# Kernel tuning notes

Measured on AMD Instinct MI355X. Metric: run time of the kernel, lower is better.

The kernel has to match this reference:

```python
import jax, jax.numpy as jnp
import numpy as np


def _chain_edges(n):
    # bidirectional chain edges + self loops (PyG GATConv add_self_loops=True default)
    src = np.concatenate([np.arange(n - 1), np.arange(1, n), np.arange(n)])
    dst = np.concatenate([np.arange(1, n), np.arange(n - 1), np.arange(n)])
    return jnp.asarray(src), jnp.asarray(dst)


def _gat(x, W, a_src, a_dst, bias, src, dst, n, heads, ch, concat):
    # x: [B, n, Fin]; PyG GATConv v1 math (lin has no bias, bias added post-agg)
    B = x.shape[0]
    xh = (x @ W).reshape(B, n, heads, ch)  # [B,n,h,c]
    es = jnp.einsum('bnhc,hc->bnh', xh, a_src)
    ed = jnp.einsum('bnhc,hc->bnh', xh, a_dst)
    e = jax.nn.leaky_relu(es[:, src] + ed[:, dst], 0.2)  # [B,E,h]
    e = jnp.moveaxis(e, 1, 0)                            # [E,B,h]
    m = jax.ops.segment_max(e, dst, num_segments=n)      # scatter-softmax over incoming edges
    w = jnp.exp(e - m[dst])
    denom = jax.ops.segment_sum(w, dst, num_segments=n)
    alpha = w / denom[dst]                               # [E,B,h]
    msgs = alpha[..., None] * jnp.moveaxis(xh[:, src], 1, 0)  # [E,B,h,c]
    out = jnp.moveaxis(jax.ops.segment_sum(msgs, dst, num_segments=n), 0, 1)  # [B,n,h,c]
    out = out.reshape(B, n, heads * ch) if concat else out.mean(axis=2)
    return out + bias


def _mlp(x, w1, b1, w2, b2, w3, b3):
    h = jax.nn.leaky_relu(x @ w1 + b1, 0.01)
    h = jax.nn.leaky_relu(h @ w2 + b2, 0.01)
    return h @ w3 + b3


def setup_inputs() -> dict:
    key = jax.random.key(0)
    ks = jax.random.split(key, 21)
    B, n, d_state, hid, da = 2048, 50, 64, 128, 4
    r = lambda k, shp, s: (jax.random.normal(k, shp, dtype=jnp.float32) * s)
    return {
        'state': r(ks[0], (B, n, d_state), 1.0),
        'W1': r(ks[1], (d_state, 2 * hid), 0.1), 'att_src1': r(ks[2], (2, hid), 0.1),
        'att_dst1': r(ks[3], (2, hid), 0.1), 'b1': r(ks[4], (2 * hid,), 0.02),
        'W2': r(ks[5], (2 * hid, hid), 0.1), 'att_src2': r(ks[6], (1, hid), 0.1),
        'att_dst2': r(ks[7], (1, hid), 0.1), 'b2': r(ks[8], (hid,), 0.02),
        'aw1': r(ks[9], (hid, 128), 0.1), 'ab1': r(ks[10], (128,), 0.02),
        'aw2': r(ks[11], (128, 128), 0.1), 'ab2': r(ks[12], (128,), 0.02),
        'aw3': r(ks[13], (128, da), 0.1), 'ab3': r(ks[14], (da,), 0.02),
        'vw1': r(ks[15], (hid, 128), 0.1), 'vb1': r(ks[16], (128,), 0.02),
        'vw2': r(ks[17], (128, 128), 0.1), 'vb2': r(ks[18], (128,), 0.02),
        'vw3': r(ks[19], (128, 1), 0.1), 'vb3': r(ks[20], (1,), 0.02),
    }


def reference(state, W1, att_src1, att_dst1, b1, W2, att_src2, att_dst2, b2,
              aw1, ab1, aw2, ab2, aw3, ab3, vw1, vb1, vw2, vb2, vw3, vb3):
    B, n, _ = state.shape
    src, dst = _chain_edges(n)
    x = jax.nn.gelu(_gat(state, W1, att_src1, att_dst1, b1, src, dst, n, 2, 128, True), approximate=False)
    x = jax.nn.gelu(_gat(x, W2, att_src2, att_dst2, b2, src, dst, n, 1, 128, False), approximate=False)
    graph_emb = x.mean(axis=1)                      # global_mean_pool over chain nodes
    value = _mlp(graph_emb, vw1, vb1, vw2, vb2, vw3, vb3)   # [B,1]
    mean = _mlp(x, aw1, ab1, aw2, ab2, aw3, ab3).reshape(B, -1)  # [B, n*d_action]
    return mean, value
```

## Files before the change

### kernel.cpp

```cpp
#include <hip/hip_runtime.h>

#define DI __device__ __forceinline__

typedef unsigned int uint32;
typedef unsigned short u16;
typedef __attribute__((ext_vector_type(8))) short s8v;
typedef __attribute__((ext_vector_type(4))) float f4v;

DI float lrelu(float x, float s){ return x > 0.f ? x : s*x; }
DI float fastrcp(float x){ float r; asm("v_rcp_f32 %0, %1" : "=v"(r) : "v"(x)); return r; }
DI u16 f2bu(float f){ uint32 u = __float_as_uint(f); return (u16)((u + 0x7FFFu + ((u>>16)&1u)) >> 16); }
DI float b16f(u16 u){ return __uint_as_float(((uint32)u)<<16); }

DI float gelu_f(float x){
  const float z = fabsf(x) * 0.70710678118654752f;
  const float t = fastrcp(1.f + 0.3275911f*z);
  float p = 1.061405429f;
  p = p*t - 1.453152027f;
  p = p*t + 1.421413741f;
  p = p*t - 0.284496736f;
  p = p*t + 0.254829592f;
  p = p*t;
  const float e = __expf(-z*z);
  float er = 1.f - p*e;
  er = copysignf(er, x);
  return 0.5f*x*(1.f + er);
}

DI f4v mfma16(s8v a, s8v b, f4v c){
  return __builtin_amdgcn_mfma_f32_16x16x32_bf16(a, b, c, 0, 0, 0);
}

constexpr int NNODE = 50;
constexpr int NT = 512;
constexpr int SCS = 266;

constexpr int WS1  = 0;
constexpr int WS2  = 17408;
constexpr int WSA1 = 54272;
constexpr int WSA2 = 70656;
constexpr int WSA3 = 87040;
constexpr int WSTOT= 89088;

__global__ __launch_bounds__(256)
void ac_prep(const float* __restrict__ w1, const float* __restrict__ as1, const float* __restrict__ ad1,
             const float* __restrict__ w2, const float* __restrict__ as2, const float* __restrict__ ad2,
             const float* __restrict__ aw1, const float* __restrict__ aw2, const float* __restrict__ aw3,
             u16* __restrict__ ws)
{
  const int T1 = 272*64, T2 = 144*256, T3 = 128*128;
  for (int t = blockIdx.x*blockDim.x + threadIdx.x; t < WSTOT; t += gridDim.x*blockDim.x){
    float v; int o;
    if (t < T1){
      int n = t>>6, k = t&63;
      if (n < 256) v = w1[k*256 + n];
      else if (n < 260){
        int sd = (n-256)>>1, h = (n-256)&1;
        const float* av = (sd ? ad1 : as1) + h*128;
        const float* wr = w1 + k*256 + h*128;
        float s = 0.f;
        for (int c=0;c<128;++c) s += wr[c]*av[c];
        v = s;
      } else v = 0.f;
      o = WS1 + n*64 + k;
    } else if (t < T1+T2){
      int j = t - T1, n = j>>8, k = j&255;
      if (n < 128) v = w2[k*128 + n];
      else if (n < 130){
        const float* av = (n==129) ? ad2 : as2;
        const float* wr = w2 + k*128;
        float s = 0.f;
        for (int c=0;c<128;++c) s += wr[c]*av[c];
        v = s;
      } else v = 0.f;
      o = WS2 + n*256 + k;
    } else if (t < T1+T2+T3){
      int j = t - T1 - T2, n = j>>7, k = j&127;
      v = aw1[k*128 + n];
      o = WSA1 + n*128 + k;
    } else if (t < T1+T2+2*T3){
      int j = t - T1 - T2 - T3, n = j>>7, k = j&127;
      v = aw2[k*128 + n];
      o = WSA2 + n*128 + k;
    } else {
      int j = t - T1 - T2 - 2*T3, m = j>>7, k = j&127;
      v = (m < 4) ? aw3[k*4 + m] : 0.f;
      o = WSA3 + m*128 + k;
    }
    ws[o] = f2bu(v);
  }
}


__global__ __launch_bounds__(NT)
void ac_main(const float* __restrict__ state,
             const float* __restrict__ b1, const float* __restrict__ b2,
             const float* __restrict__ ab1, const float* __restrict__ ab2,
             const float* __restrict__ ab3,
             const float* __restrict__ vw1, const float* __restrict__ vb1,
             const float* __restrict__ vw2, const float* __restrict__ vb2,
             const float* __restrict__ vw3, const float* __restrict__ vb3,
             const u16* __restrict__ ws,
             float* __restrict__ out_mean, float* __restrict__ out_val)
{
  __shared__ __align__(16) float sm[19828];
  u16*   pAb  = (u16*)sm;
  u16*   pAs  = (u16*)sm;
  float* gebP = sm + 3200;
  float* vh1  = sm + 3712;
  float* sc   = sm + 6400;
  u16*   pAb2 = (u16*)(sm + 6400);
  float* geb  = sm + 19700;

  const int tid = threadIdx.x, b = blockIdx.x;
  const int wid = tid>>6, l15 = tid&15, g = (tid>>4)&3;

  {
    const float4* xb4 = (const float4*)(state + (size_t)b * (NNODE*64));
    for (int t = tid; t < 800; t += NT){
      float4 v = xb4[t];
      int i = t>>4, k0 = (t&15)*4;
      ushort4 u;
      u.x = f2bu(v.x); u.y = f2bu(v.y); u.z = f2bu(v.z); u.w = f2bu(v.w);
      *(ushort4*)(pAs + i*64 + (k0 ^ ((i&7)<<3))) = u;
    }
  }
  __syncthreads();

  s8v aS[4][2];
  #pragma unroll
  for (int mt=0;mt<4;++mt)
    #pragma unroll
    for (int ks=0;ks<2;++ks){
      int row = mt*16 + l15, c = ks*32 + g*8;
      aS[mt][ks] = *(const s8v*)(pAs + row*64 + (c ^ ((row&7)<<3)));
    }

  for (int nt = wid; nt < 17; nt += 8){
    f4v acc[4];
    #pragma unroll
    for (int mt=0;mt<4;++mt) acc[mt] = (f4v){0.f,0.f,0.f,0.f};
    #pragma unroll
    for (int ks=0;ks<2;++ks){
      s8v bf = *(const s8v*)(ws + WS1 + (nt*16 + l15)*64 + ks*32 + g*8);
      #pragma unroll
      for (int mt=0;mt<4;++mt) acc[mt] = mfma16(aS[mt][ks], bf, acc[mt]);
    }
    const int col = nt*16 + l15;
    if (col < 260){
      #pragma unroll
      for (int mt=0;mt<4;++mt){
        #pragma unroll
        for (int r=0;r<4;++r){
          const int row = mt*16 + g*4 + r;
          if (mt < 3 || row < NNODE) sc[row*SCS + col] = acc[mt][r];
        }
      }
    }
  }
  __syncthreads();

  {
    const int i = tid & 63;
    if (i < NNODE){
      #pragma unroll
      for (int h=0;h<2;++h){
        const float edi = sc[i*SCS + 258 + h];
        const float eS = __expf(lrelu(sc[i*SCS + 256 + h] + edi, 0.2f));
        const float eL = (i > 0)       ? __expf(lrelu(sc[(i-1)*SCS + 256 + h] + edi, 0.2f)) : 0.f;
        const float eR = (i < NNODE-1) ? __expf(lrelu(sc[(i+1)*SCS + 256 + h] + edi, 0.2f)) : 0.f;
        const float rs = fastrcp(eL + eS + eR);
        sc[i*SCS + 260 + h*3    ] = eL*rs;
        sc[i*SCS + 260 + h*3 + 1] = eS*rs;
        sc[i*SCS + 260 + h*3 + 2] = eR*rs;
      }
    }
  }
  {
    const int q = tid>>8, j = tid&255, h = j>>7;
    const int i0 = q*25, i1 = i0 + 25;
    const float bj = b1[j];
    const int wc = 260 + h*3;
    float pv  = (i0 > 0) ? sc[(i0-1)*SCS + j] : 0.f;
    float cur = sc[i0*SCS + j];
    #pragma unroll 5
    for (int i = i0; i < i1; ++i){
      const float nx = (i < NNODE-1) ? sc[(i+1)*SCS + j] : 0.f;
      const float wL = sc[i*SCS + wc], wS = sc[i*SCS + wc + 1], wR = sc[i*SCS + wc + 2];
      const float v = gelu_f(wL*pv + wS*cur + wR*nx + bj);
      pAb[i*256 + (j ^ ((i&7)<<3))] = f2bu(v);
      pv = cur; cur = nx;
    }
  }
  __syncthreads();

  for (int nt = wid; nt < 9; nt += 8){
    f4v acc[4];
    #pragma unroll
    for (int mt=0;mt<4;++mt) acc[mt] = (f4v){0.f,0.f,0.f,0.f};
    #pragma unroll
    for (int ks=0;ks<8;++ks){
      s8v bf = *(const s8v*)(ws + WS2 + (nt*16 + l15)*256 + ks*32 + g*8);
      #pragma unroll
      for (int mt=0;mt<4;++mt){
        const int row = mt*16 + l15, c = ks*32 + g*8;
        s8v a = *(const s8v*)(pAb + row*256 + (c ^ ((row&7)<<3)));
        acc[mt] = mfma16(a, bf, acc[mt]);
      }
    }
    const int col = nt*16 + l15;
    if (col < 130){
      #pragma unroll
      for (int mt=0;mt<4;++mt){
        #pragma unroll
        for (int r=0;r<4;++r){
          const int row = mt*16 + g*4 + r;
          if (mt < 3 || row < NNODE) sc[row*SCS + col] = acc[mt][r];
        }
      }
    }
  }
  __syncthreads();

  {
    const int i = tid & 63;
    if (i < NNODE){
      const float edi = sc[i*SCS + 129];
      const float eS = __expf(lrelu(sc[i*SCS + 128] + edi, 0.2f));
      const float eL = (i > 0)       ? __expf(lrelu(sc[(i-1)*SCS + 128] + edi, 0.2f)) : 0.f;
      const float eR = (i < NNODE-1) ? __expf(lrelu(sc[(i+1)*SCS + 128] + edi, 0.2f)) : 0.f;
      const float rs = fastrcp(eL + eS + eR);
      sc[i*SCS + 130] = eL*rs;
      sc[i*SCS + 131] = eS*rs;
      sc[i*SCS + 132] = eR*rs;
    }
  }
  {
    const int q = tid>>7, j = tid&127;
    const int i0 = q*13, i1 = (i0+13 < NNODE) ? i0+13 : NNODE;
    const float bj = b2[j];
    float ps = 0.f;
    float pv  = (i0 > 0) ? sc[(i0-1)*SCS + j] : 0.f;
    float cur = sc[i0*SCS + j];
    #pragma unroll 4
    for (int i = i0; i < i1; ++i){
      const float nx = (i < NNODE-1) ? sc[(i+1)*SCS + j] : 0.f;
      const float wL = sc[i*SCS + 130], wS = sc[i*SCS + 131], wR = sc[i*SCS + 132];
      const float v = gelu_f(wL*pv + wS*cur + wR*nx + bj);
      pAb[i*128 + (j ^ ((i&7)<<3))] = f2bu(v);
      ps += v;
      pv = cur; cur = nx;
    }
    gebP[q*128 + j] = ps;
  }
  __syncthreads();

  {
    const int nt = wid;
    f4v acc[4];
    #pragma unroll
    for (int mt=0;mt<4;++mt) acc[mt] = (f4v){0.f,0.f,0.f,0.f};
    #pragma unroll
    for (int ks=0;ks<4;++ks){
      s8v bf = *(const s8v*)(ws + WSA1 + (nt*16 + l15)*128 + ks*32 + g*8);
      #pragma unroll
      for (int mt=0;mt<4;++mt){
        const int row = mt*16 + l15, c = ks*32 + g*8;
        s8v a = *(const s8v*)(pAb + row*128 + (c ^ ((row&7)<<3)));
        acc[mt] = mfma16(a, bf, acc[mt]);
      }
    }
    const int col = nt*16 + l15;
    const float bj = ab1[col];
    #pragma unroll
    for (int mt=0;mt<4;++mt){
      #pragma unroll
      for (int r=0;r<4;++r){
        const int row = mt*16 + g*4 + r;
        if (mt < 3 || row < NNODE){
          const float v = lrelu(acc[mt][r] + bj, 0.01f);
          pAb2[row*128 + (col ^ ((row&7)<<3))] = f2bu(v);
        }
      }
    }
    if (tid < 128)
      geb[tid] = (gebP[tid] + gebP[128+tid] + gebP[256+tid] + gebP[384+tid]) * 0.02f;
  }
  __syncthreads();

  {
    const int nt = wid;
    f4v acc[4];
    #pragma unroll
    for (int mt=0;mt<4;++mt) acc[mt] = (f4v){0.f,0.f,0.f,0.f};
    #pragma unroll
    for (int ks=0;ks<4;++ks){
      s8v bf = *(const s8v*)(ws + WSA2 + (nt*16 + l15)*128 + ks*32 + g*8);
      #pragma unroll
      for (int mt=0;mt<4;++mt){
        const int row = mt*16 + l15, c = ks*32 + g*8;
        s8v a = *(const s8v*)(pAb2 + row*128 + (c ^ ((row&7)<<3)));
        acc[mt] = mfma16(a, bf, acc[mt]);
      }
    }
    const int col = nt*16 + l15;
    const float bj = ab2[col];
    #pragma unroll
    for (int mt=0;mt<4;++mt){
      #pragma unroll
      for (int r=0;r<4;++r){
        const int row = mt*16 + g*4 + r;
        if (mt < 3 || row < NNODE){
          const float v = lrelu(acc[mt][r] + bj, 0.01f);
          pAb[row*128 + (col ^ ((row&7)<<3))] = f2bu(v);
        }
      }
    }
  }
  __syncthreads();

  if (wid < 4){
    const int mt = wid;
    f4v acc = (f4v){0.f,0.f,0.f,0.f};
    #pragma unroll
    for (int ks=0;ks<4;++ks){
      s8v bf = *(const s8v*)(ws + WSA3 + l15*128 + ks*32 + g*8);
      const int row = mt*16 + l15, c = ks*32 + g*8;
      s8v a = *(const s8v*)(pAb + row*128 + (c ^ ((row&7)<<3)));
      acc = mfma16(a, bf, acc);
    }
    if (l15 < 4){
      const float bj = ab3[l15];
      #pragma unroll
      for (int r=0;r<4;++r){
        const int row = mt*16 + g*4 + r;
        if (row < NNODE) out_mean[(size_t)b*200 + row*4 + l15] = acc[r] + bj;
      }
    }
  } else if (wid == 4){
    const int j = tid & 63;
    float a0=0.f, a1=0.f;
    #pragma unroll 4
    for (int k=0;k<128;++k){
      const float gk = geb[k];
      a0 += gk*vw1[k*128 + j];
      a1 += gk*vw1[k*128 + j + 64];
    }
    vh1[j]      = lrelu(a0 + vb1[j],    0.01f);
    vh1[j + 64] = lrelu(a1 + vb1[j+64], 0.01f);
    asm volatile("s_waitcnt lgkmcnt(0)" ::: "memory");
    __builtin_amdgcn_sched_barrier(0);
    float c0=0.f, c1=0.f;
    #pragma unroll 4
    for (int k=0;k<128;++k){
      const float hk = vh1[k];
      c0 += hk*vw2[k*128 + j];
      c1 += hk*vw2[k*128 + j + 64];
    }
    const float va = lrelu(c0 + vb2[j],    0.01f);
    const float vb = lrelu(c1 + vb2[j+64], 0.01f);
    float p = va*vw3[j] + vb*vw3[j+64];
    #pragma unroll
    for (int off=32; off>0; off>>=1) p += __shfl_down(p, off);
    if (j == 0) out_val[b] = p + vb3[0];
  }
}

extern "C" void kernel_launch(void* const* d_in, const int* in_sizes, int n_in,
                              void* d_out, int out_size, void* d_ws, size_t ws_size,
                              hipStream_t stream)
{
  const float* state = (const float*)d_in[0];
  const float* w1    = (const float*)d_in[1];
  const float* as1   = (const float*)d_in[2];
  const float* ad1   = (const float*)d_in[3];
  const float* b1_   = (const float*)d_in[4];
  const float* w2    = (const float*)d_in[5];
  const float* as2   = (const float*)d_in[6];
  const float* ad2   = (const float*)d_in[7];
  const float* b2_   = (const float*)d_in[8];
  const float* aw1   = (const float*)d_in[9];
  const float* ab1   = (const float*)d_in[10];
  const float* aw2   = (const float*)d_in[11];
  const float* ab2   = (const float*)d_in[12];
  const float* aw3   = (const float*)d_in[13];
  const float* ab3   = (const float*)d_in[14];
  const float* vw1   = (const float*)d_in[15];
  const float* vb1   = (const float*)d_in[16];
  const float* vw2   = (const float*)d_in[17];
  const float* vb2   = (const float*)d_in[18];
  const float* vw3   = (const float*)d_in[19];
  const float* vb3   = (const float*)d_in[20];

  const int B = in_sizes[0] / (NNODE * 64);
  float* out_mean = (float*)d_out;
  float* out_val  = out_mean + (size_t)B * 200;
  u16* ws = (u16*)d_ws;

  ac_prep<<<128, 256, 0, stream>>>(w1, as1, ad1, w2, as2, ad2, aw1, aw2, aw3, ws);
  ac_main<<<B, NT, 0, stream>>>(state, b1_, b2_, ab1, ab2, ab3,
                                vw1, vb1, vw2, vb2, vw3, vb3,
                                ws, out_mean, out_val);
}
```

Before: 140.7 us.

## Make GAT attention and aggregation wave-local to drop block barriers

Every wave now computes the attention-score column tile itself, alongside its own feature tiles. The softmax weights and the neighbour aggregation then only need intra-wave LDS waits instead of block-wide __syncthreads. The input state is converted to bf16 straight into MFMA registers, skipping the LDS staging pass and its barrier. The layer-2 mean pool is reduced with shuffles, and the layer-2 output is packed into unused score-buffer columns, with the row stride padded for alignment. The cost is redundant attention-tile MFMAs in each wave and identical values written concurrently to shared LDS slots.

Measured after the change: 178.8 us. 27.1% more time.

```diff
diff --git a/kernel.cpp b/kernel.cpp
--- a/kernel.cpp
+++ b/kernel.cpp
@@ -33,7 +33,7 @@
 
 constexpr int NNODE = 50;
 constexpr int NT = 512;
-constexpr int SCS = 266;
+constexpr int SCS = 268;
 
 constexpr int WS1  = 0;
 constexpr int WS2  = 17408;
@@ -103,40 +103,44 @@
              const u16* __restrict__ ws,
              float* __restrict__ out_mean, float* __restrict__ out_val)
 {
-  __shared__ __align__(16) float sm[19828];
-  u16*   pAb  = (u16*)sm;
-  u16*   pAs  = (u16*)sm;
-  float* gebP = sm + 3200;
-  float* vh1  = sm + 3712;
-  float* sc   = sm + 6400;
-  u16*   pAb2 = (u16*)(sm + 6400);
-  float* geb  = sm + 19700;
+  __shared__ __align__(16) float sm[20056];
+  u16*   pA2 = (u16*)sm;
+  u16*   pA4 = (u16*)sm;
+  u16*   pA5 = (u16*)(sm + 3200);
+  float* sc  = sm + 6400;
+  float* geb = sm + 19800;
+  float* vh1 = sm + 19928;
 
   const int tid = threadIdx.x, b = blockIdx.x;
   const int wid = tid>>6, l15 = tid&15, g = (tid>>4)&3;
-
+  const int lan = tid & 63, lc = lan & 15, lq = lan >> 4;
+
+  s8v aS[4][2];
   {
-    const float4* xb4 = (const float4*)(state + (size_t)b * (NNODE*64));
-    for (int t = tid; t < 800; t += NT){
-      float4 v = xb4[t];
-      int i = t>>4, k0 = (t&15)*4;
-      ushort4 u;
-      u.x = f2bu(v.x); u.y = f2bu(v.y); u.z = f2bu(v.z); u.w = f2bu(v.w);
-      *(ushort4*)(pAs + i*64 + (k0 ^ ((i&7)<<3))) = u;
-    }
-  }
-  __syncthreads();
-
-  s8v aS[4][2];
+    const float* xb = state + (size_t)b * (NNODE*64);
+    #pragma unroll
+    for (int mt=0;mt<4;++mt){
+      const int row = mt*16 + l15;
+      #pragma unroll
+      for (int ks=0;ks<2;++ks){
+        union { s8v v; u16 u[8]; } fr;
+        if (mt < 3 || row < NNODE){
+          const float* p = xb + row*64 + ks*32 + g*8;
+          const float4 f0 = *(const float4*)(p);
+          const float4 f1 = *(const float4*)(p + 4);
+          fr.u[0]=f2bu(f0.x); fr.u[1]=f2bu(f0.y); fr.u[2]=f2bu(f0.z); fr.u[3]=f2bu(f0.w);
+          fr.u[4]=f2bu(f1.x); fr.u[5]=f2bu(f1.y); fr.u[6]=f2bu(f1.z); fr.u[7]=f2bu(f1.w);
+        } else {
+          fr.u[0]=fr.u[1]=fr.u[2]=fr.u[3]=fr.u[4]=fr.u[5]=fr.u[6]=fr.u[7]=0;
+        }
+        aS[mt][ks] = fr.v;
+      }
+    }
+  }
+
   #pragma unroll
-  for (int mt=0;mt<4;++mt)
-    #pragma unroll
-    for (int ks=0;ks<2;++ks){
-      int row = mt*16 + l15, c = ks*32 + g*8;
-      aS[mt][ks] = *(const s8v*)(pAs + row*64 + (c ^ ((row&7)<<3)));
-    }
-
-  for (int nt = wid; nt < 17; nt += 8){
+  for (int tt=0; tt<3; ++tt){
+    const int nt = (tt < 2) ? (wid + tt*8) : 16;
     f4v acc[4];
     #pragma unroll
     for (int mt=0;mt<4;++mt) acc[mt] = (f4v){0.f,0.f,0.f,0.f};
@@ -158,43 +162,50 @@
       }
     }
   }
+  asm volatile("s_waitcnt lgkmcnt(0)" ::: "memory");
+  __builtin_amdgcn_sched_barrier(0);
+
+  if (lan < NNODE){
+    const int i = lan;
+    #pragma unroll
+    for (int h=0;h<2;++h){
+      const float edi = sc[i*SCS + 258 + h];
+      const float eS = __expf(lrelu(sc[i*SCS + 256 + h] + edi, 0.2f));
+      const float eL = (i > 0)       ? __expf(lrelu(sc[(i-1)*SCS + 256 + h] + edi, 0.2f)) : 0.f;
+      const float eR = (i < NNODE-1) ? __expf(lrelu(sc[(i+1)*SCS + 256 + h] + edi, 0.2f)) : 0.f;
+      const float rs = fastrcp(eL + eS + eR);
+      sc[i*SCS + 260 + h*3    ] = eL*rs;
+      sc[i*SCS + 260 + h*3 + 1] = eS*rs;
+      sc[i*SCS + 260 + h*3 + 2] = eR*rs;
+    }
+  }
+  asm volatile("s_waitcnt lgkmcnt(0)" ::: "memory");
+  __builtin_amdgcn_sched_barrier(0);
+
+  {
+    const int i0 = lq*13, i1 = (i0+13 < NNODE) ? i0+13 : NNODE;
+    #pragma unroll
+    for (int cb=0; cb<2; ++cb){
+      const int col = (wid + cb*8)*16 + lc;
+      const int wc = 260 + (col >> 7)*3;
+      const float bj = b1[col];
+      float pv  = (i0 > 0) ? sc[(i0-1)*SCS + col] : 0.f;
+      float cur = sc[i0*SCS + col];
+      #pragma unroll 4
+      for (int i=i0; i<i1; ++i){
+        const float nx = (i < NNODE-1) ? sc[(i+1)*SCS + col] : 0.f;
+        const float wL = sc[i*SCS + wc], wS = sc[i*SCS + wc+1], wR = sc[i*SCS + wc+2];
+        const float v = gelu_f(wL*pv + wS*cur + wR*nx + bj);
+        pA2[i*256 + (col ^ ((i&7)<<3))] = f2bu(v);
+        pv = cur; cur = nx;
+      }
+    }
+  }
   __syncthreads();
 
-  {
-    const int i = tid & 63;
-    if (i < NNODE){
-      #pragma unroll
-      for (int h=0;h<2;++h){
-        const float edi = sc[i*SCS + 258 + h];
-        const float eS = __expf(lrelu(sc[i*SCS + 256 + h] + edi, 0.2f));
-        const float eL = (i > 0)       ? __expf(lrelu(sc[(i-1)*SCS + 256 + h] + edi, 0.2f)) : 0.f;
-        const float eR = (i < NNODE-1) ? __expf(lrelu(sc[(i+1)*SCS + 256 + h] + edi, 0.2f)) : 0.f;
-        const float rs = fastrcp(eL + eS + eR);
-        sc[i*SCS + 260 + h*3    ] = eL*rs;
-        sc[i*SCS + 260 + h*3 + 1] = eS*rs;
-        sc[i*SCS + 260 + h*3 + 2] = eR*rs;
-      }
-    }
-  }
-  {
-    const int q = tid>>8, j = tid&255, h = j>>7;
-    const int i0 = q*25, i1 = i0 + 25;
-    const float bj = b1[j];
-    const int wc = 260 + h*3;
-    float pv  = (i0 > 0) ? sc[(i0-1)*SCS + j] : 0.f;
-    float cur = sc[i0*SCS + j];
-    #pragma unroll 5
-    for (int i = i0; i < i1; ++i){
-      const float nx = (i < NNODE-1) ? sc[(i+1)*SCS + j] : 0.f;
-      const float wL = sc[i*SCS + wc], wS = sc[i*SCS + wc + 1], wR = sc[i*SCS + wc + 2];
-      const float v = gelu_f(wL*pv + wS*cur + wR*nx + bj);
-      pAb[i*256 + (j ^ ((i&7)<<3))] = f2bu(v);
-      pv = cur; cur = nx;
-    }
-  }
-  __syncthreads();
-
-  for (int nt = wid; nt < 9; nt += 8){
+  #pragma unroll
+  for (int tt=0; tt<2; ++tt){
+    const int nt = tt ? 8 : wid;
     f4v acc[4];
     #pragma unroll
     for (int mt=0;mt<4;++mt) acc[mt] = (f4v){0.f,0.f,0.f,0.f};
@@ -204,7 +215,7 @@
       #pragma unroll
       for (int mt=0;mt<4;++mt){
         const int row = mt*16 + l15, c = ks*32 + g*8;
-        s8v a = *(const s8v*)(pAb + row*256 + (c ^ ((row&7)<<3)));
+        s8v a = *(const s8v*)(pA2 + row*256 + (c ^ ((row&7)<<3)));
         acc[mt] = mfma16(a, bf, acc[mt]);
       }
     }
@@ -220,43 +231,48 @@
       }
     }
   }
-  __syncthreads();
+  asm volatile("s_waitcnt lgkmcnt(0)" ::: "memory");
+  __builtin_amdgcn_sched_barrier(0);
+
+  if (lan < NNODE){
+    const int i = lan;
+    const float edi = sc[i*SCS + 129];
+    const float eS = __expf(lrelu(sc[i*SCS + 128] + edi, 0.2f));
+    const float eL = (i > 0)       ? __expf(lrelu(sc[(i-1)*SCS + 128] + edi, 0.2f)) : 0.f;
+    const float eR = (i < NNODE-1) ? __expf(lrelu(sc[(i+1)*SCS + 128] + edi, 0.2f)) : 0.f;
+    const float rs = fastrcp(eL + eS + eR);
+    sc[i*SCS + 130] = eL*rs;
+    sc[i*SCS + 131] = eS*rs;
+    sc[i*SCS + 132] = eR*rs;
+  }
+  asm volatile("s_waitcnt lgkmcnt(0)" ::: "memory");
+  __builtin_amdgcn_sched_barrier(0);
 
   {
-    const int i = tid & 63;
-    if (i < NNODE){
-      const float edi = sc[i*SCS + 129];
-      const float eS = __expf(lrelu(sc[i*SCS + 128] + edi, 0.2f));
-      const float eL = (i > 0)       ? __expf(lrelu(sc[(i-1)*SCS + 128] + edi, 0.2f)) : 0.f;
-      const float eR = (i < NNODE-1) ? __expf(lrelu(sc[(i+1)*SCS + 128] + edi, 0.2f)) : 0.f;
-      const float rs = fastrcp(eL + eS + eR);
-      sc[i*SCS + 130] = eL*rs;
-      sc[i*SCS + 131] = eS*rs;
-      sc[i*SCS + 132] = eR*rs;
-    }
-  }
-  {
-    const int q = tid>>7, j = tid&127;
-    const int i0 = q*13, i1 = (i0+13 < NNODE) ? i0+13 : NNODE;
-    const float bj = b2[j];
+    const int col = wid*16 + lc;
+    const int i0 = lq*13, i1 = (i0+13 < NNODE) ? i0+13 : NNODE;
+    const float bj = b2[col];
     float ps = 0.f;
-    float pv  = (i0 > 0) ? sc[(i0-1)*SCS + j] : 0.f;
-    float cur = sc[i0*SCS + j];
+    float pv  = (i0 > 0) ? sc[(i0-1)*SCS + col] : 0.f;
+    float cur = sc[i0*SCS + col];
     #pragma unroll 4
-    for (int i = i0; i < i1; ++i){
-      const float nx = (i < NNODE-1) ? sc[(i+1)*SCS + j] : 0.f;
+    for (int i=i0; i<i1; ++i){
+      const float nx = (i < NNODE-1) ? sc[(i+1)*SCS + col] : 0.f;
       const float wL = sc[i*SCS + 130], wS = sc[i*SCS + 131], wR = sc[i*SCS + 132];
       const float v = gelu_f(wL*pv + wS*cur + wR*nx + bj);
-      pAb[i*128 + (j ^ ((i&7)<<3))] = f2bu(v);
+      ((u16*)(sc + i*SCS + 140))[col ^ ((i&7)<<3)] = f2bu(v);
       ps += v;
       pv = cur; cur = nx;
     }
-    gebP[q*128 + j] = ps;
+    ps += __shfl_xor(ps, 16);
+    ps += __shfl_xor(ps, 32);
+    if (lq == 0) geb[col] = ps * 0.02f;
   }
   __syncthreads();
 
   {
     const int nt = wid;
+    const s8v zv = {0,0,0,0,0,0,0,0};
     f4v acc[4];
     #pragma unroll
     for (int mt=0;mt<4;++mt) acc[mt] = (f4v){0.f,0.f,0.f,0.f};
@@ -266,7 +282,9 @@
       #pragma unroll
       for (int mt=0;mt<4;++mt){
         const int row = mt*16 + l15, c = ks*32 + g*8;
-        s8v a = *(const s8v*)(pAb + row*128 + (c ^ ((row&7)<<3)));
+        s8v a = zv;
+        if (mt < 3 || row < NNODE)
+          a = *(const s8v*)((const u16*)(sc + row*SCS + 140) + (c ^ ((row&7)<<3)));
         acc[mt] = mfma16(a, bf, acc[mt]);
       }
     }
@@ -279,12 +297,10 @@
         const int row = mt*16 + g*4 + r;
         if (mt < 3 || row < NNODE){
           const float v = lrelu(acc[mt][r] + bj, 0.01f);
-          pAb2[row*128 + (col ^ ((row&7)<<3))] = f2bu(v);
+          pA4[row*128 + (col ^ ((row&7)<<3))] = f2bu(v);
         }
       }
     }
-    if (tid < 128)
-      geb[tid] = (gebP[tid] + gebP[128+tid] + gebP[256+tid] + gebP[384+tid]) * 0.02f;
   }
   __syncthreads();
 
@@ -299,7 +315,7 @@
       #pragma unroll
       for (int mt=0;mt<4;++mt){
         const int row = mt*16 + l15, c = ks*32 + g*8;
-        s8v a = *(const s8v*)(pAb2 + row*128 + (c ^ ((row&7)<<3)));
+        s8v a = *(const s8v*)(pA4 + row*128 + (c ^ ((row&7)<<3)));
         acc[mt] = mfma16(a, bf, acc[mt]);
       }
     }
@@ -312,7 +328,7 @@
         const int row = mt*16 + g*4 + r;
         if (mt < 3 || row < NNODE){
           const float v = lrelu(acc[mt][r] + bj, 0.01f);
-          pAb[row*128 + (col ^ ((row&7)<<3))] = f2bu(v);
+          pA5[row*128 + (col ^ ((row&7)<<3))] = f2bu(v);
         }
       }
     }
@@ -326,7 +342,7 @@
     for (int ks=0;ks<4;++ks){
       s8v bf = *(const s8v*)(ws + WSA3 + l15*128 + ks*32 + g*8);
       const int row = mt*16 + l15, c = ks*32 + g*8;
-      s8v a = *(const s8v*)(pAb + row*128 + (c ^ ((row&7)<<3)));
+      s8v a = *(const s8v*)(pA5 + row*128 + (c ^ ((row&7)<<3)));
       acc = mfma16(a, bf, acc);
     }
     if (l15 < 4){
@@ -338,7 +354,7 @@
       }
     }
   } else if (wid == 4){
-    const int j = tid & 63;
+    const int j = lan;
     float a0=0.f, a1=0.f;
     #pragma unroll 4
     for (int k=0;k<128;++k){
```
